# Kernel tuning notes

Hardware: AMD Instinct MI355X
Metric: run time of the kernel (lower is better)

## Reference

```python
import jax, jax.numpy as jnp
import numpy as np

LN_EPS = 1e-5

def layer_norm(x, g, b):
    mu = jnp.mean(x, axis=-1, keepdims=True)
    var = jnp.mean(jnp.square(x - mu), axis=-1, keepdims=True)
    return (x - mu) * jax.lax.rsqrt(var + LN_EPS) * g + b

def ternary_quant(w):
    # BitNet b1.58-style ternary quantization with straight-through estimator
    scale = 1.0 / jnp.clip(jnp.mean(jnp.abs(w)), 1e-5)
    wq = jnp.clip(jnp.round(w * scale), -1.0, 1.0) / scale
    return w + jax.lax.stop_gradient(wq - w)

def setup_inputs() -> dict:
    key = jax.random.key(0)
    ks = jax.random.split(key, 3)
    dim, hidden = 1024, 4096
    B, S = 8, 1024
    x = jax.random.normal(ks[0], (B, S, dim), dtype=jnp.float32)
    w1 = jax.random.normal(ks[1], (hidden, dim), dtype=jnp.float32) * 0.02
    w2 = jax.random.normal(ks[2], (dim, hidden), dtype=jnp.float32) * 0.02
    return {
        "x": x,
        "ln1_g": jnp.ones((dim,), jnp.float32), "ln1_b": jnp.zeros((dim,), jnp.float32),
        "w1": w1, "b1": jnp.zeros((hidden,), jnp.float32),
        "ln2_g": jnp.ones((hidden,), jnp.float32), "ln2_b": jnp.zeros((hidden,), jnp.float32),
        "w2": w2, "b2": jnp.zeros((dim,), jnp.float32),
    }

def reference(x, ln1_g, ln1_b, w1, b1, ln2_g, ln2_b, w2, b2):
    h = layer_norm(x, ln1_g, ln1_b)
    h = jnp.einsum('bsd,hd->bsh', h, ternary_quant(w1)) + b1  # [B,S,hidden]
    h = jax.nn.gelu(h, approximate=False)  # nn.GELU default is exact erf
    h = layer_norm(h, ln2_g, ln2_b)
    out = jnp.einsum('bsh,dh->bsd', h, ternary_quant(w2)) + b2  # [B,S,dim]
    return out
```

## Files before the change

kernel.cpp:

```cpp
#include <hip/hip_runtime.h>
#include <cstdint>
#include <cstddef>

#define DIM   1024
#define HID   4096
#define MROWS 8192

typedef __attribute__((ext_vector_type(8))) __bf16 bf16x8;
typedef __attribute__((ext_vector_type(4))) float  f32x4;

__device__ __forceinline__ unsigned short f2bf(float f) {
  unsigned int u = __float_as_uint(f);
  u += 0x7fffu + ((u >> 16) & 1u);
  return (unsigned short)(u >> 16);
}
__device__ __forceinline__ float bf2f(unsigned int lo16) {
  return __uint_as_float(lo16 << 16);
}

__device__ __forceinline__ float fast_gelu(float v) {
  float u = v * (0.79788456080286536f + 0.035677408136300125f * v * v);
  float e = __builtin_amdgcn_exp2f(u * 2.8853900817779268f);
  float r = __builtin_amdgcn_rcpf(e + 1.0f);
  return v - v * r;
}

__device__ __forceinline__ void gld16(const void* g, void* l) {
  auto* gp = reinterpret_cast<__attribute__((address_space(1))) unsigned int*>(
      reinterpret_cast<uintptr_t>(g));
  auto* lp = reinterpret_cast<__attribute__((address_space(3))) unsigned int*>(
      reinterpret_cast<uintptr_t>(l));
  __builtin_amdgcn_global_load_lds(gp, lp, 16, 0, 0);
}

__device__ __forceinline__ void wave_reduce2(float& a, float& b) {
#pragma unroll
  for (int off = 32; off > 0; off >>= 1) {
    a += __shfl_xor(a, off, 64);
    b += __shfl_xor(b, off, 64);
  }
}

__device__ __forceinline__ void block_reduce2(float& a, float& b, int tid) {
  __shared__ float red[8];
  __syncthreads();
  wave_reduce2(a, b);
  if ((tid & 63) == 0) { red[tid >> 6] = a; red[4 + (tid >> 6)] = b; }
  __syncthreads();
  a = red[0] + red[1] + red[2] + red[3];
  b = red[4] + red[5] + red[6] + red[7];
}

__global__ __launch_bounds__(256)
void prep_kernel(const float* __restrict__ w1, const float* __restrict__ w2,
                 float* __restrict__ part,
                 const float* __restrict__ x, const float* __restrict__ g,
                 const float* __restrict__ b, unsigned short* __restrict__ xn) {
  int tid = threadIdx.x;
  int bid = blockIdx.x;
  if (bid < 2048) {
    const float* w = (bid < 1024) ? w1 : w2;
    int blk = bid & 1023;
    const float4* base = (const float4*)w + (size_t)blk * 1024;
    float s = 0.f;
#pragma unroll
    for (int i = 0; i < 4; ++i) {
      float4 v = base[tid + i * 256];
      s += fabsf(v.x) + fabsf(v.y) + fabsf(v.z) + fabsf(v.w);
    }
#pragma unroll
    for (int off = 32; off > 0; off >>= 1) s += __shfl_xor(s, off, 64);
    __shared__ float red[4];
    if ((tid & 63) == 0) red[tid >> 6] = s;
    __syncthreads();
    if (tid == 0) part[bid] = red[0] + red[1] + red[2] + red[3];
  } else {
    const int row  = (bid - 2048) * 4 + (tid >> 6);
    const int lane = tid & 63;
    const float4* xr = (const float4*)(x + (size_t)row * DIM);
    const float4* g4 = (const float4*)g;
    const float4* b4 = (const float4*)b;
    float4 v[4];
    float s = 0.f, ss = 0.f;
#pragma unroll
    for (int p = 0; p < 4; ++p) {
      v[p] = xr[lane + 64 * p];
      s  += v[p].x + v[p].y + v[p].z + v[p].w;
      ss += v[p].x * v[p].x + v[p].y * v[p].y + v[p].z * v[p].z + v[p].w * v[p].w;
    }
    wave_reduce2(s, ss);
    float mu  = s * (1.0f / DIM);
    float var = ss * (1.0f / DIM) - mu * mu;
    float rs  = rsqrtf(var + 1e-5f);
    uint2* dst = (uint2*)(xn + (size_t)row * DIM);
#pragma unroll
    for (int p = 0; p < 4; ++p) {
      float4 gg = g4[lane + 64 * p];
      float4 bb = b4[lane + 64 * p];
      uint2 r;
      r.x = (unsigned)f2bf((v[p].x - mu) * rs * gg.x + bb.x) |
            ((unsigned)f2bf((v[p].y - mu) * rs * gg.y + bb.y) << 16);
      r.y = (unsigned)f2bf((v[p].z - mu) * rs * gg.z + bb.z) |
            ((unsigned)f2bf((v[p].w - mu) * rs * gg.w + bb.w) << 16);
      dst[lane + 64 * p] = r;
    }
  }
}

__global__ __launch_bounds__(256)
void quant_kernel(const float* __restrict__ part,
                  const float* __restrict__ w1, unsigned short* __restrict__ q1,
                  const float* __restrict__ w2, unsigned short* __restrict__ q2,
                  const float* __restrict__ g2, const float* __restrict__ b2,
                  const float* __restrict__ bias2,
                  float* __restrict__ Sg, float* __restrict__ Cb,
                  float* __restrict__ scal) {
  int bid = blockIdx.x, tid = threadIdx.x;
  const int lane = tid & 63;
  const float4* psrc = (const float4*)(part + ((bid < 512) ? 0 : 1024));
  float a = 0.f, dummy = 0.f;
#pragma unroll
  for (int p = 0; p < 4; ++p) {
    float4 pv = psrc[lane + 64 * p];
    a += pv.x + pv.y + pv.z + pv.w;
  }
  wave_reduce2(a, dummy);
  float mean = fmaxf(a * (1.0f / 4194304.0f), 1e-5f);
  float sc = 1.0f / mean;

  if (bid < 512) {
    if (bid == 0 && tid == 0) scal[0] = mean;
    const int n4 = 1048576;
    int i = bid * 256 + tid;
    for (; i < n4; i += 512 * 256) {
      float4 v = ((const float4*)w1)[i];
      float t0 = fminf(fmaxf(rintf(v.x * sc), -1.f), 1.f);
      float t1 = fminf(fmaxf(rintf(v.y * sc), -1.f), 1.f);
      float t2 = fminf(fmaxf(rintf(v.z * sc), -1.f), 1.f);
      float t3 = fminf(fmaxf(rintf(v.w * sc), -1.f), 1.f);
      uint2 r;
      r.x = (unsigned)f2bf(t0) | ((unsigned)f2bf(t1) << 16);
      r.y = (unsigned)f2bf(t2) | ((unsigned)f2bf(t3) << 16);
      ((uint2*)q1)[i] = r;
    }
  } else {
    const int d = bid - 512;
    if (d == 0 && tid == 0) scal[1] = mean;
    const float4* wr = (const float4*)(w2 + (size_t)d * HID);
    const float4* g4 = (const float4*)g2;
    const float4* b4 = (const float4*)b2;
    uint2* qr = (uint2*)(q2 + (size_t)d * HID);
    float s1 = 0.f, s2 = 0.f;
#pragma unroll
    for (int i = 0; i < 4; ++i) {
      int idx = tid + 256 * i;
      float4 wv = wr[idx], gv = g4[idx], bv = b4[idx];
      float t0 = fminf(fmaxf(rintf(wv.x * sc), -1.f), 1.f);
      float t1 = fminf(fmaxf(rintf(wv.y * sc), -1.f), 1.f);
      float t2 = fminf(fmaxf(rintf(wv.z * sc), -1.f), 1.f);
      float t3 = fminf(fmaxf(rintf(wv.w * sc), -1.f), 1.f);
      s1 += gv.x * t0 + gv.y * t1 + gv.z * t2 + gv.w * t3;
      s2 += bv.x * t0 + bv.y * t1 + bv.z * t2 + bv.w * t3;
      uint2 r;
      r.x = (unsigned)f2bf(t0 * gv.x) | ((unsigned)f2bf(t1 * gv.y) << 16);
      r.y = (unsigned)f2bf(t2 * gv.z) | ((unsigned)f2bf(t3 * gv.w) << 16);
      qr[idx] = r;
    }
    block_reduce2(s1, s2, tid);
    if (tid == 0) {
      Sg[d] = mean * s1;
      Cb[d] = mean * s2 + bias2[d];
    }
  }
}

__global__ __launch_bounds__(256)
void rowstats_kernel(const unsigned short* __restrict__ h,
                     const float* __restrict__ meanp,
                     float2* __restrict__ murs) {
  const int row  = blockIdx.x * 4 + (threadIdx.x >> 6);
  const int lane = threadIdx.x & 63;
  const uint4* hr = (const uint4*)(h + (size_t)row * HID);
  float s = 0.f, ss = 0.f;
#pragma unroll
  for (int p = 0; p < 8; ++p) {
    uint4 pk = hr[lane + 64 * p];
    const unsigned int* pu = (const unsigned int*)&pk;
#pragma unroll
    for (int j = 0; j < 4; ++j) {
      float lo = bf2f(pu[j] & 0xffffu);
      float hi = __uint_as_float(pu[j] & 0xffff0000u);
      s += lo + hi; ss += lo * lo + hi * hi;
    }
  }
  wave_reduce2(s, ss);
  if (lane == 0) {
    float mu  = s * (1.0f / HID);
    float var = ss * (1.0f / HID) - mu * mu;
    float rs  = rsqrtf(var + 1e-5f);
    murs[row] = make_float2(rs * meanp[1], -rs * mu);
  }
}

template <int MODE, int MT, int KK>
__global__ __launch_bounds__(256)
void gemm_bt(const unsigned short* __restrict__ A,
             const unsigned short* __restrict__ B,
             void* __restrict__ Cv,
             const float* __restrict__ wscale_ptr,
             const float* __restrict__ bias,
             const float2* __restrict__ murs,
             const float* __restrict__ Sg,
             const float* __restrict__ Cb,
             int N) {
  constexpr int IT = MT / 32;
  __shared__ unsigned short sA[MT * 64];
  __shared__ unsigned short sB[128 * 64];

  const int tid  = threadIdx.x;
  const int lane = tid & 63;
  const int wave = tid >> 6;
  const int wm   = wave & 1;
  const int wn   = wave >> 1;

  const int nbx  = gridDim.x;
  const int id   = blockIdx.y * nbx + blockIdx.x;
  const int xcd  = id & 7;
  const int slot = id >> 3;
  const int bandsPerXcd = gridDim.y >> 3;
  const int band = xcd * bandsPerXcd + slot / nbx;
  const int col  = slot - (slot / nbx) * nbx;
  const int bm   = band * MT;
  const int bn   = col * 128;

  const int csw = (((tid & 7) ^ ((tid >> 3) & 7))) * 8;
  const unsigned short* Ab = A + (size_t)(bm + (tid >> 3)) * KK + csw;
  const unsigned short* Bb = B + (size_t)(bn + (tid >> 3)) * KK + csw;

  f32x4 acc[IT][4] = {};

  const int rowA = (wm * (MT / 2) + (lane & 15)) * 64;
  const int rowB = (wn * 64 + (lane & 15)) * 64;
  const int p0 = ((0 + (lane >> 4)) ^ (lane & 7)) * 8;
  const int p1 = ((4 + (lane >> 4)) ^ (lane & 7)) * 8;

  for (int k0 = 0; k0 < KK; k0 += 64) {
#pragma unroll
    for (int i = 0; i < IT; ++i)
      gld16(Ab + (size_t)(32 * i) * KK + k0, sA + i * 2048 + tid * 8);
#pragma unroll
    for (int i = 0; i < 4; ++i)
      gld16(Bb + (size_t)(32 * i) * KK + k0, sB + i * 2048 + tid * 8);
    __syncthreads();

#pragma unroll
    for (int h = 0; h < 2; ++h) {
      const int ph = h ? p1 : p0;
      bf16x8 af[IT], bfr[4];
#pragma unroll
      for (int i = 0; i < IT; ++i) af[i] = *(const bf16x8*)(sA + rowA + i * 1024 + ph);
#pragma unroll
      for (int j = 0; j < 4; ++j) bfr[j] = *(const bf16x8*)(sB + rowB + j * 1024 + ph);
#pragma unroll
      for (int i = 0; i < IT; ++i)
#pragma unroll
        for (int j = 0; j < 4; ++j)
          acc[i][j] = __builtin_amdgcn_mfma_f32_16x16x32_bf16(af[i], bfr[j], acc[i][j], 0, 0, 0);
    }
    __syncthreads();
  }

  if (MODE == 1) {
    const float wscale = *wscale_ptr;
    float bv[4];
#pragma unroll
    for (int j = 0; j < 4; ++j) bv[j] = bias[bn + wn * 64 + j * 16 + (lane & 15)];
#pragma unroll
    for (int i = 0; i < IT; ++i) {
      const int m0 = bm + wm * (MT / 2) + i * 16 + ((lane >> 4) << 2);
#pragma unroll
      for (int j = 0; j < 4; ++j) {
        const int n = bn + wn * 64 + j * 16 + (lane & 15);
#pragma unroll
        for (int r = 0; r < 4; ++r) {
          float v = fast_gelu(acc[i][j][r] * wscale + bv[j]);
          ((unsigned short*)Cv)[(size_t)(m0 + r) * N + n] = f2bf(v);
        }
      }
    }
  } else {
    float sg[4], cb[4];
#pragma unroll
    for (int j = 0; j < 4; ++j) {
      const int n = bn + wn * 64 + j * 16 + (lane & 15);
      sg[j] = Sg[n];
      cb[j] = Cb[n];
    }
#pragma unroll
    for (int i = 0; i < IT; ++i) {
      const int m0 = bm + wm * (MT / 2) + i * 16 + ((lane >> 4) << 2);
#pragma unroll
      for (int r = 0; r < 4; ++r) {
        float2 ab = murs[m0 + r];
#pragma unroll
        for (int j = 0; j < 4; ++j) {
          const int n = bn + wn * 64 + j * 16 + (lane & 15);
          ((float*)Cv)[(size_t)(m0 + r) * N + n] = ab.x * acc[i][j][r] + ab.y * sg[j] + cb[j];
        }
      }
    }
  }
}

extern "C" void kernel_launch(void* const* d_in, const int* in_sizes, int n_in,
                              void* d_out, int out_size, void* d_ws, size_t ws_size,
                              hipStream_t stream) {
  const float* x     = (const float*)d_in[0];
  const float* g1    = (const float*)d_in[1];
  const float* b1v   = (const float*)d_in[2];
  const float* w1    = (const float*)d_in[3];
  const float* bias1 = (const float*)d_in[4];
  const float* g2    = (const float*)d_in[5];
  const float* b2v   = (const float*)d_in[6];
  const float* w2    = (const float*)d_in[7];
  const float* bias2 = (const float*)d_in[8];
  float* out = (float*)d_out;

  char* ws = (char*)d_ws;
  float* scal          = (float*)ws;
  float* part          = (float*)(ws + 64);
  unsigned short* q1   = (unsigned short*)(ws + 16384);
  unsigned short* q2   = q1 + 4194304;
  unsigned short* xn   = q2 + 4194304;
  unsigned short* h    = xn + 8388608;
  float2* murs         = (float2*)(h + 33554432);
  float* Sg            = (float*)(murs + 8192);
  float* Cb            = Sg + 1024;

  prep_kernel<<<4096, 256, 0, stream>>>(w1, w2, part, x, g1, b1v, xn);
  quant_kernel<<<1536, 256, 0, stream>>>(part, w1, q1, w2, q2, g2, b2v, bias2, Sg, Cb, scal);
  gemm_bt<1, 128, DIM><<<dim3(HID / 128, MROWS / 128), 256, 0, stream>>>(
      xn, q1, h, scal + 0, bias1, nullptr, nullptr, nullptr, HID);
  rowstats_kernel<<<2048, 256, 0, stream>>>(h, scal, murs);
  gemm_bt<0, 64, HID><<<dim3(DIM / 128, MROWS / 64), 256, 0, stream>>>(
      h, q2, out, scal + 1, nullptr, murs, Sg, Cb, DIM);
}
```

Before: 288.4 us.

## Quantize LN1 activations to int8 and run first GEMM with int8 MFMA

The first layer norm now emits per-row absmax-scaled int8 activations plus a per-row inverse scale, and the ternary w1 weights are stored as int8 instead of bf16. A new int8 GEMM kernel built on 16x16x64 i8 MFMA replaces the bf16 GEMM for the first projection. Its epilogue rescales the int32 accumulators, adds bias and applies GELU. This halves operand bytes and uses the higher int8 MFMA rate, at the cost of activation quantization error against the bf16 path. The new kernel has no double buffering, and its epilogue writes scalar bf16 stores with a strided pattern.

```diff
diff --git a/kernel.cpp b/kernel.cpp
--- a/kernel.cpp
+++ b/kernel.cpp
@@ -8,6 +8,7 @@
 
 typedef __attribute__((ext_vector_type(8))) __bf16 bf16x8;
 typedef __attribute__((ext_vector_type(4))) float  f32x4;
+typedef __attribute__((ext_vector_type(4))) int    i32x4;
 
 __device__ __forceinline__ unsigned short f2bf(float f) {
   unsigned int u = __float_as_uint(f);
@@ -39,6 +40,11 @@
     a += __shfl_xor(a, off, 64);
     b += __shfl_xor(b, off, 64);
   }
+}
+__device__ __forceinline__ float wave_reduce_max(float m) {
+#pragma unroll
+  for (int off = 32; off > 0; off >>= 1) m = fmaxf(m, __shfl_xor(m, off, 64));
+  return m;
 }
 
 __device__ __forceinline__ void block_reduce2(float& a, float& b, int tid) {
@@ -55,7 +61,8 @@
 void prep_kernel(const float* __restrict__ w1, const float* __restrict__ w2,
                  float* __restrict__ part,
                  const float* __restrict__ x, const float* __restrict__ g,
-                 const float* __restrict__ b, unsigned short* __restrict__ xn) {
+                 const float* __restrict__ b, unsigned int* __restrict__ xn8,
+                 float* __restrict__ invs) {
   int tid = threadIdx.x;
   int bid = blockIdx.x;
   if (bid < 2048) {
@@ -92,16 +99,33 @@
     float mu  = s * (1.0f / DIM);
     float var = ss * (1.0f / DIM) - mu * mu;
     float rs  = rsqrtf(var + 1e-5f);
-    uint2* dst = (uint2*)(xn + (size_t)row * DIM);
+    float n[4][4];
+    float amax = 0.f;
 #pragma unroll
     for (int p = 0; p < 4; ++p) {
       float4 gg = g4[lane + 64 * p];
       float4 bb = b4[lane + 64 * p];
-      uint2 r;
-      r.x = (unsigned)f2bf((v[p].x - mu) * rs * gg.x + bb.x) |
-            ((unsigned)f2bf((v[p].y - mu) * rs * gg.y + bb.y) << 16);
-      r.y = (unsigned)f2bf((v[p].z - mu) * rs * gg.z + bb.z) |
-            ((unsigned)f2bf((v[p].w - mu) * rs * gg.w + bb.w) << 16);
+      n[p][0] = (v[p].x - mu) * rs * gg.x + bb.x;
+      n[p][1] = (v[p].y - mu) * rs * gg.y + bb.y;
+      n[p][2] = (v[p].z - mu) * rs * gg.z + bb.z;
+      n[p][3] = (v[p].w - mu) * rs * gg.w + bb.w;
+#pragma unroll
+      for (int c = 0; c < 4; ++c) amax = fmaxf(amax, fabsf(n[p][c]));
+    }
+    amax = wave_reduce_max(amax);
+    float sc, iv;
+    if (amax < 1e-20f) { sc = 0.f; iv = 0.f; }
+    else               { sc = 127.0f / amax; iv = amax * (1.0f / 127.0f); }
+    if (lane == 0) invs[row] = iv;
+    unsigned int* dst = xn8 + (size_t)row * 256;
+#pragma unroll
+    for (int p = 0; p < 4; ++p) {
+      unsigned r = 0;
+#pragma unroll
+      for (int c = 0; c < 4; ++c) {
+        int q = (int)rintf(n[p][c] * sc);
+        r |= ((unsigned)q & 0xffu) << (8 * c);
+      }
       dst[lane + 64 * p] = r;
     }
   }
@@ -109,7 +133,7 @@
 
 __global__ __launch_bounds__(256)
 void quant_kernel(const float* __restrict__ part,
-                  const float* __restrict__ w1, unsigned short* __restrict__ q1,
+                  const float* __restrict__ w1, unsigned int* __restrict__ q1,
                   const float* __restrict__ w2, unsigned short* __restrict__ q2,
                   const float* __restrict__ g2, const float* __restrict__ b2,
                   const float* __restrict__ bias2,
@@ -134,14 +158,13 @@
     int i = bid * 256 + tid;
     for (; i < n4; i += 512 * 256) {
       float4 v = ((const float4*)w1)[i];
-      float t0 = fminf(fmaxf(rintf(v.x * sc), -1.f), 1.f);
-      float t1 = fminf(fmaxf(rintf(v.y * sc), -1.f), 1.f);
-      float t2 = fminf(fmaxf(rintf(v.z * sc), -1.f), 1.f);
-      float t3 = fminf(fmaxf(rintf(v.w * sc), -1.f), 1.f);
-      uint2 r;
-      r.x = (unsigned)f2bf(t0) | ((unsigned)f2bf(t1) << 16);
-      r.y = (unsigned)f2bf(t2) | ((unsigned)f2bf(t3) << 16);
-      ((uint2*)q1)[i] = r;
+      int t0 = (int)fminf(fmaxf(rintf(v.x * sc), -1.f), 1.f);
+      int t1 = (int)fminf(fmaxf(rintf(v.y * sc), -1.f), 1.f);
+      int t2 = (int)fminf(fmaxf(rintf(v.z * sc), -1.f), 1.f);
+      int t3 = (int)fminf(fmaxf(rintf(v.w * sc), -1.f), 1.f);
+      unsigned r = ((unsigned)t0 & 0xffu) | (((unsigned)t1 & 0xffu) << 8) |
+                   (((unsigned)t2 & 0xffu) << 16) | (((unsigned)t3 & 0xffu) << 24);
+      q1[i] = r;
     }
   } else {
     const int d = bid - 512;
@@ -199,6 +222,84 @@
     float var = ss * (1.0f / HID) - mu * mu;
     float rs  = rsqrtf(var + 1e-5f);
     murs[row] = make_float2(rs * meanp[1], -rs * mu);
+  }
+}
+
+__global__ __launch_bounds__(256)
+void gemm1_i8(const unsigned char* __restrict__ A,
+              const unsigned char* __restrict__ B,
+              unsigned short* __restrict__ H,
+              const float* __restrict__ wscale_ptr,
+              const float* __restrict__ invs,
+              const float* __restrict__ bias) {
+  __shared__ unsigned char sA[128 * 64];
+  __shared__ unsigned char sB[128 * 64];
+
+  const int tid  = threadIdx.x;
+  const int lane = tid & 63;
+  const int wave = tid >> 6;
+  const int wm   = wave & 1;
+  const int wn   = wave >> 1;
+
+  const int nbx  = gridDim.x;
+  const int id   = blockIdx.y * nbx + blockIdx.x;
+  const int xcd  = id & 7;
+  const int slot = id >> 3;
+  const int bandsPerXcd = gridDim.y >> 3;
+  const int band = xcd * bandsPerXcd + slot / nbx;
+  const int col  = slot - (slot / nbx) * nbx;
+  const int bm   = band * 128;
+  const int bn   = col * 128;
+
+  const int csw = ((tid & 3) ^ ((tid >> 3) & 3)) * 16;
+  const unsigned char* Ab = A + (size_t)(bm + (tid >> 2)) * 1024 + csw;
+  const unsigned char* Bb = B + (size_t)(bn + (tid >> 2)) * 1024 + csw;
+
+  i32x4 acc[4][4] = {};
+
+  const int rowA = (wm * 64 + (lane & 15)) * 64;
+  const int rowB = (wn * 64 + (lane & 15)) * 64;
+  const int kc = (((lane >> 4) ^ ((lane >> 1) & 3))) * 16;
+
+  for (int k0 = 0; k0 < 1024; k0 += 64) {
+    gld16(Ab + k0,              sA + tid * 16);
+    gld16(Ab + 64 * 1024 + k0,  sA + 4096 + tid * 16);
+    gld16(Bb + k0,              sB + tid * 16);
+    gld16(Bb + 64 * 1024 + k0,  sB + 4096 + tid * 16);
+    __syncthreads();
+
+    i32x4 af[4], bfr[4];
+#pragma unroll
+    for (int i = 0; i < 4; ++i) af[i]  = *(const i32x4*)(sA + rowA + i * 1024 + kc);
+#pragma unroll
+    for (int j = 0; j < 4; ++j) bfr[j] = *(const i32x4*)(sB + rowB + j * 1024 + kc);
+#pragma unroll
+    for (int i = 0; i < 4; ++i)
+#pragma unroll
+      for (int j = 0; j < 4; ++j)
+        acc[i][j] = __builtin_amdgcn_mfma_i32_16x16x64_i8(af[i], bfr[j], acc[i][j], 0, 0, 0);
+    __syncthreads();
+  }
+
+  const float wscale = *wscale_ptr;
+  float bv[4];
+#pragma unroll
+  for (int j = 0; j < 4; ++j) bv[j] = bias[bn + wn * 64 + j * 16 + (lane & 15)];
+#pragma unroll
+  for (int i = 0; i < 4; ++i) {
+    const int m0 = bm + wm * 64 + i * 16 + ((lane >> 4) << 2);
+    float asc[4];
+#pragma unroll
+    for (int r = 0; r < 4; ++r) asc[r] = wscale * invs[m0 + r];
+#pragma unroll
+    for (int j = 0; j < 4; ++j) {
+      const int n = bn + wn * 64 + j * 16 + (lane & 15);
+#pragma unroll
+      for (int r = 0; r < 4; ++r) {
+        float v = fast_gelu((float)acc[i][j][r] * asc[r] + bv[j]);
+        H[(size_t)(m0 + r) * HID + n] = f2bf(v);
+      }
+    }
   }
 }
 
@@ -329,18 +430,19 @@
   char* ws = (char*)d_ws;
   float* scal          = (float*)ws;
   float* part          = (float*)(ws + 64);
-  unsigned short* q1   = (unsigned short*)(ws + 16384);
-  unsigned short* q2   = q1 + 4194304;
-  unsigned short* xn   = q2 + 4194304;
-  unsigned short* h    = xn + 8388608;
-  float2* murs         = (float2*)(h + 33554432);
+  float* invs          = (float*)(ws + 16384);
+  unsigned int* q1     = (unsigned int*)(ws + 65536);
+  unsigned short* q2   = (unsigned short*)(ws + 65536 + 4194304);
+  unsigned int* xn8    = (unsigned int*)((char*)q2 + 8388608);
+  unsigned short* h    = (unsigned short*)((char*)xn8 + 8388608);
+  float2* murs         = (float2*)((char*)h + 67108864);
   float* Sg            = (float*)(murs + 8192);
   float* Cb            = Sg + 1024;
 
-  prep_kernel<<<4096, 256, 0, stream>>>(w1, w2, part, x, g1, b1v, xn);
+  prep_kernel<<<4096, 256, 0, stream>>>(w1, w2, part, x, g1, b1v, xn8, invs);
   quant_kernel<<<1536, 256, 0, stream>>>(part, w1, q1, w2, q2, g2, b2v, bias2, Sg, Cb, scal);
-  gemm_bt<1, 128, DIM><<<dim3(HID / 128, MROWS / 128), 256, 0, stream>>>(
-      xn, q1, h, scal + 0, bias1, nullptr, nullptr, nullptr, HID);
+  gemm1_i8<<<dim3(HID / 128, MROWS / 128), 256, 0, stream>>>(
+      (const unsigned char*)xn8, (const unsigned char*)q1, h, scal + 0, invs, bias1);
   rowstats_kernel<<<2048, 256, 0, stream>>>(h, scal, murs);
   gemm_bt<0, 64, HID><<<dim3(DIM / 128, MROWS / 64), 256, 0, stream>>>(
       h, q2, out, scal + 1, nullptr, murs, Sg, Cb, DIM);
```

Result: faster. 262.4 us (-9.0%).
